# Kernel optimization log

Hardware: AMD Instinct MI355X
Metric: run time of the kernel (lower is better)

## Reference

```python
import jax, jax.numpy as jnp
import numpy as np

DT_SCALER = 1.0 / 24
COVAR_INDEX = np.array([0] + list(range(7, 25)))
INSULIN_INDEX = np.array(list(range(1, 6)))
T = 100          # SEQUENCE_LENGTH
B = 512
H = 256          # hidden_dim
ODE_H = 50       # hidden width of the ODE MLP (hardcoded in cODERNN_)
ODE_STEPS = 8    # fixed-step RK4 stands in for adaptive dopri5 (rtol=atol=1e-3)


def setup_inputs() -> dict:
    key = jax.random.key(0)
    ks = jax.random.split(key, 24)
    std = 0.1
    d = {}
    d["dt"] = jax.random.uniform(ks[0], (B, T, 2), jnp.float32)
    d["x"] = jax.random.normal(ks[1], (B, T, 25), jnp.float32)
    # rnn1: RNNCell(19, H)
    d["Wih1"] = std * jax.random.normal(ks[2], (H, 19), jnp.float32)
    d["Whh1"] = std * jax.random.normal(ks[3], (H, H), jnp.float32)
    d["bih1"] = jnp.zeros((H,), jnp.float32)
    d["bhh1"] = jnp.zeros((H,), jnp.float32)
    # rnn2: RNNCell(5+H, H)
    d["Wih2"] = std * jax.random.normal(ks[4], (H, 5 + H), jnp.float32)
    d["Whh2"] = std * jax.random.normal(ks[5], (H, H), jnp.float32)
    d["bih2"] = jnp.zeros((H,), jnp.float32)
    d["bhh2"] = jnp.zeros((H,), jnp.float32)
    # output_net_covar: Linear(H,H) -> tanh -> Linear(H,1)
    d["oW1"] = std * jax.random.normal(ks[6], (H, H), jnp.float32)
    d["ob1"] = jnp.zeros((H,), jnp.float32)
    d["oW2"] = std * jax.random.normal(ks[7], (1, H), jnp.float32)
    d["ob2"] = jnp.zeros((1,), jnp.float32)
    # output_net_insulin: Linear(H,H) -> tanh -> Linear(H,1) -> relu
    d["iW1"] = std * jax.random.normal(ks[8], (H, H), jnp.float32)
    d["ib1"] = jnp.zeros((H,), jnp.float32)
    d["iW2"] = std * jax.random.normal(ks[9], (1, H), jnp.float32)
    d["ib2"] = jnp.zeros((1,), jnp.float32)
    # ODE func net: Linear(H,50) -> tanh -> Linear(50,H)
    d["fW1"] = std * jax.random.normal(ks[10], (ODE_H, H), jnp.float32)
    d["fb1"] = jnp.zeros((ODE_H,), jnp.float32)
    d["fW2"] = std * jax.random.normal(ks[11], (H, ODE_H), jnp.float32)
    d["fb2"] = jnp.zeros((H,), jnp.float32)
    return d


def _rnn_cell(x, h, Wih, Whh, bih, bhh):
    return jnp.tanh(x @ Wih.T + bih + h @ Whh.T + bhh)


def _solve_ode(h0, scale, fW1, fb1, fW2, fb2):
    """Integrate dh/ds = net(h) * scale over s in [0,1] with fixed-step RK4.
    scale = dt_i * DT_SCALER, shape [B,1]."""
    hs = 1.0 / ODE_STEPS

    def f(h):
        return (jnp.tanh(h @ fW1.T + fb1) @ fW2.T + fb2) * scale

    def step(h, _):
        k1 = f(h)
        k2 = f(h + 0.5 * hs * k1)
        k3 = f(h + 0.5 * hs * k2)
        k4 = f(h + hs * k3)
        return h + (hs / 6.0) * (k1 + 2 * k2 + 2 * k3 + k4), None

    h, _ = jax.lax.scan(step, h0, None, length=ODE_STEPS)
    return h


def reference(dt, x, Wih1, Whh1, bih1, bhh1, Wih2, Whh2, bih2, bhh2,
              oW1, ob1, oW2, ob2, iW1, ib1, iW2, ib2, fW1, fb1, fW2, fb2):
    Bb, Tt, _ = x.shape
    x_ins = x[:, :, INSULIN_INDEX]      # [B,T,5]
    x_cov = x[:, :, COVAR_INDEX]        # [B,T,19]
    treat = (jnp.sum(x_ins > 0, axis=2, keepdims=True) > 0).astype(x.dtype)  # [B,T,1]
    dt_i = (dt[:, :, 1] - dt[:, :, 0])[..., None]                            # [B,T,1]

    def out_cov(h):
        return jnp.tanh(h @ oW1.T + ob1) @ oW2.T + ob2

    def out_ins(h):
        return jax.nn.relu(jnp.tanh(h @ iW1.T + ib1) @ iW2.T + ib2)

    def step(carry, inp):
        h_cov, h_ins = carry
        xc, xi, d, tr = inp             # [B,19],[B,5],[B,1],[B,1]
        h_cov = h_cov + _rnn_cell(xc, h_cov, Wih1, Whh1, bih1, bhh1)
        h_ins = h_ins + _rnn_cell(jnp.concatenate([xi, h_cov], axis=1), h_ins,
                                  Wih2, Whh2, bih2, bhh2)
        scale = d * DT_SCALER
        h_cov = _solve_ode(h_cov, scale, fW1, fb1, fW2, fb2)
        h_ins = _solve_ode(h_ins, scale, fW1, fb1, fW2, fb2)
        mu = out_cov(h_cov) - tr * out_ins(h_ins)   # [B,1]
        return (h_cov, h_ins), mu

    Hd = Whh1.shape[0]
    init = (jnp.zeros((Bb, Hd), x.dtype), jnp.zeros((Bb, Hd), x.dtype))
    xs = (jnp.swapaxes(x_cov, 0, 1), jnp.swapaxes(x_ins, 0, 1),
          jnp.swapaxes(dt_i, 0, 1), jnp.swapaxes(treat, 0, 1))
    _, mus = jax.lax.scan(step, init, xs)           # [T,B,1]
    return jnp.swapaxes(mus[:, :, 0], 0, 1)        # [B,T]
```

## Files before the change

### kernel.cpp

```cpp
#include <hip/hip_runtime.h>

#define TT 100
#define NSTEP 8
__device__ __constant__ float kDT_SC = 1.0f / 24.0f;
#define HS (0.125f)

typedef float f4 __attribute__((ext_vector_type(4)));
typedef float f2 __attribute__((ext_vector_type(2)));

#define OFF_WHH1T4   0
#define OFF_WIH1T    65536
#define OFF_WIH2AT   70656
#define OFF_WIH2BT4  72704
#define OFF_WHH2T4   138240
#define OFF_OW1T4    203776
#define OFF_IW1T4    269312
#define OFF_FW1R     334848
#define OFF_FW2T4    351232
#define OFF_B1C      364544
#define OFF_B2C      364800
#define WS_FLOATS    365056

#define L_FW2   0
#define L_YCUR  13312
#define L_Z     13856
#define L_HC2   13984
#define L_XA    14240
#define L_TR    14268
#define L_RED   14269
#define L_TOTAL 14277

__device__ __forceinline__ float fast_tanh(float v) {
    float e = __expf(2.0f * v);
    return 1.0f - 2.0f / (e + 1.0f);
}
__device__ __forceinline__ f2 vlo(f4 v) { return __builtin_shufflevector(v, v, 0, 1); }
__device__ __forceinline__ f2 vhi(f4 v) { return __builtin_shufflevector(v, v, 2, 3); }
__device__ __forceinline__ void pkfma(f2& a, f2 w, f2 h) {
    a = __builtin_elementwise_fma(w, h, a);
}
__device__ __forceinline__ float rsum2(f2 a) { return a.x + a.y; }

__device__ __forceinline__ int yoffF(int v, int j) { return v * 272 + (j >> 6) * 68 + (j & 63); }
__device__ __forceinline__ int yoff4(int v, int jb) { return v * 68 + (jb >> 4) * 17 + (jb & 15); }

template <int CTRL>
__device__ __forceinline__ float dpp_rr_add(float v) {
    int r = __builtin_amdgcn_update_dpp(0, __float_as_int(v), CTRL, 0xF, 0xF, false);
    return v + __int_as_float(r);
}
__device__ __forceinline__ float allreduce16(float v) {
    v = dpp_rr_add<0x121>(v);
    v = dpp_rr_add<0x122>(v);
    v = dpp_rr_add<0x124>(v);
    v = dpp_rr_add<0x128>(v);
    return v;
}

__global__ void codernn_setup(const float* __restrict__ Wih1, const float* __restrict__ Whh1,
                              const float* __restrict__ bih1, const float* __restrict__ bhh1,
                              const float* __restrict__ Wih2, const float* __restrict__ Whh2,
                              const float* __restrict__ bih2, const float* __restrict__ bhh2,
                              const float* __restrict__ oW1, const float* __restrict__ iW1,
                              const float* __restrict__ fW1, const float* __restrict__ fW2,
                              float* __restrict__ ws) {
    int e = blockIdx.x * 256 + threadIdx.x;
    if (e >= WS_FLOATS) return;
    float v;
    if (e < OFF_WIH1T) {
        int q = e; int jb = q >> 10, i = (q >> 2) & 255, dj = q & 3;
        v = Whh1[i * 256 + jb * 4 + dj];
    } else if (e < OFF_WIH2AT) {
        int q = e - OFF_WIH1T; int j = q >> 8, i = q & 255;
        v = (j < 19) ? Wih1[i * 19 + j] : 0.0f;
    } else if (e < OFF_WIH2BT4) {
        int q = e - OFF_WIH2AT; int j = q >> 8, i = q & 255;
        v = (j < 5) ? Wih2[i * 261 + j] : 0.0f;
    } else if (e < OFF_WHH2T4) {
        int q = e - OFF_WIH2BT4; int jb = q >> 10, i = (q >> 2) & 255, dj = q & 3;
        v = Wih2[i * 261 + 5 + jb * 4 + dj];
    } else if (e < OFF_OW1T4) {
        int q = e - OFF_WHH2T4; int jb = q >> 10, i = (q >> 2) & 255, dj = q & 3;
        v = Whh2[i * 256 + jb * 4 + dj];
    } else if (e < OFF_IW1T4) {
        int q = e - OFF_OW1T4; int jb = q >> 10, i = (q >> 2) & 255, dj = q & 3;
        v = oW1[i * 256 + jb * 4 + dj];
    } else if (e < OFF_FW1R) {
        int q = e - OFF_IW1T4; int jb = q >> 10, i = (q >> 2) & 255, dj = q & 3;
        v = iW1[i * 256 + jb * 4 + dj];
    } else if (e < OFF_FW2T4) {
        int q = e - OFF_FW1R; int k = q >> 8, j = q & 255;
        v = (k < 50) ? fW1[k * 256 + j] : 0.0f;
    } else if (e < OFF_B1C) {
        int q = e - OFF_FW2T4; int kb = q >> 10, i = (q >> 2) & 255, dk = q & 3;
        int k = kb * 4 + dk;
        v = (k < 50) ? fW2[i * 50 + k] : 0.0f;
    } else if (e < OFF_B2C) {
        int q = e - OFF_B1C; v = bih1[q] + bhh1[q];
    } else {
        int q = e - OFF_B2C; v = bih2[q] + bhh2[q];
    }
    ws[e] = v;
}

__global__ __launch_bounds__(256, 2) void codernn_main(
    const float* __restrict__ dt, const float* __restrict__ x,
    const float* __restrict__ ws,
    const float* __restrict__ ob1, const float* __restrict__ oW2, const float* __restrict__ ob2,
    const float* __restrict__ ib1, const float* __restrict__ iW2, const float* __restrict__ ib2,
    const float* __restrict__ fb1, const float* __restrict__ fb2,
    float* __restrict__ out) {
    __shared__ float sm[L_TOTAL];
    const int tid = threadIdx.x;
    const int i = tid;
    const int bg = blockIdx.x;
    const int lane = tid & 63, wv = tid >> 6;

    for (int idx = tid; idx < 13312; idx += 256) sm[L_FW2 + idx] = ws[OFF_FW2T4 + idx];
    for (int idx = tid; idx < 544; idx += 256) sm[L_YCUR + idx] = 0.0f;

    const float b1ci = ws[OFF_B1C + i];
    const float b2ci = ws[OFF_B2C + i];
    const float ob1i = ob1[i], ib1i = ib1[i];
    const float oW2i = oW2[i], iW2i = iW2[i];
    const float fb2i = fb2[i];
    const float ob2s = ob2[0], ib2s = ib2[0];

    const int kg = (tid >> 4) & 15;
    const int p16 = tid & 15;

    const f4* Whh1T4  = (const f4*)(ws + OFF_WHH1T4);
    const float* Wih1T  = ws + OFF_WIH1T;
    const float* Wih2aT = ws + OFF_WIH2AT;
    const f4* Wih2bT4 = (const f4*)(ws + OFF_WIH2BT4);
    const f4* Whh2T4  = (const f4*)(ws + OFF_WHH2T4);
    const f4* oW1T4   = (const f4*)(ws + OFF_OW1T4);
    const f4* iW1T4   = (const f4*)(ws + OFF_IW1T4);
    const f4* ycur4   = (const f4*)(sm + L_YCUR);
    const f4* hc24    = (const f4*)(sm + L_HC2);
    const f4* fw2l    = (const f4*)(sm + L_FW2);

    f4 wz[4][4];
    {
        const f4* g = (const f4*)(ws + OFF_FW1R);
        #pragma unroll
        for (int r = 0; r < 4; ++r)
            #pragma unroll
            for (int m = 0; m < 4; ++m)
                wz[r][m] = g[(4 * kg + r) * 64 + p16 * 4 + m];
    }
    float fb1r[4];
    #pragma unroll
    for (int r = 0; r < 4; ++r) fb1r[r] = (4 * kg + r < 50) ? fb1[4 * kg + r] : 0.0f;

    const int yA = L_YCUR + yoffF(0, i);
    const int yB = L_YCUR + yoffF(1, i);

    float y0a = 0.0f, y0b = 0.0f;
    __syncthreads();

    for (int t = 0; t < TT; ++t) {
        if (tid < 28) {
            sm[L_XA + tid] = (tid < 25) ? x[bg * (TT * 25) + t * 25 + tid] : 0.0f;
        }
        if (i == 0) {
            const float* xp = x + bg * (TT * 25) + t * 25;
            sm[L_TR] = (xp[1] > 0.f || xp[2] > 0.f || xp[3] > 0.f || xp[4] > 0.f || xp[5] > 0.f) ? 1.0f : 0.0f;
        }
        const float sc = (dt[bg * (TT * 2) + t * 2 + 1] - dt[bg * (TT * 2) + t * 2]) * kDT_SC;
        __syncthreads();

        {
            float acc = b1ci;
            acc = fmaf(Wih1T[i], sm[L_XA + 0], acc);
            #pragma unroll
            for (int j = 1; j < 19; ++j)
                acc = fmaf(Wih1T[j * 256 + i], sm[L_XA + 6 + j], acc);
            f2 aL = {0.f, 0.f}, aH = {0.f, 0.f};
            #pragma unroll 4
            for (int jb = 0; jb < 64; ++jb) {
                f4 w = Whh1T4[jb * 256 + i];
                f4 h = ycur4[yoff4(0, jb)];
                pkfma(aL, vlo(w), vlo(h));
                pkfma(aH, vhi(w), vhi(h));
            }
            acc += rsum2(aL + aH);
            y0a = y0a + fast_tanh(acc);
            sm[L_HC2 + i] = y0a;
        }
        __syncthreads();

        {
            float acc = b2ci;
            #pragma unroll
            for (int j = 0; j < 5; ++j)
                acc = fmaf(Wih2aT[j * 256 + i], sm[L_XA + 1 + j], acc);
            f2 aL = {0.f, 0.f}, aH = {0.f, 0.f};
            #pragma unroll 4
            for (int jb = 0; jb < 64; ++jb) {
                f4 w = Wih2bT4[jb * 256 + i];
                f4 h = hc24[jb];
                pkfma(aL, vlo(w), vlo(h));
                pkfma(aH, vhi(w), vhi(h));
            }
            #pragma unroll 4
            for (int jb = 0; jb < 64; ++jb) {
                f4 w = Whh2T4[jb * 256 + i];
                f4 h = ycur4[yoff4(1, jb)];
                pkfma(aL, vlo(w), vlo(h));
                pkfma(aH, vhi(w), vhi(h));
            }
            acc += rsum2(aL + aH);
            y0b = y0b + fast_tanh(acc);
        }
        __syncthreads();
        sm[yA] = y0a;
        sm[yB] = y0b;

        for (int st = 0; st < NSTEP; ++st) {
            float acca = 0.f, accb = 0.f;
            #pragma unroll
            for (int e = 0; e < 4; ++e) {
                __syncthreads();
                float pz[8];
                #pragma unroll
                for (int s = 0; s < 2; ++s) {
                    const f4* ys = ycur4 + s * 68 + (p16 >> 2) * 17 + (p16 & 3) * 4;
                    f2 P0l = {0,0}, P0h = {0,0}, P1l = {0,0}, P1h = {0,0};
                    f2 P2l = {0,0}, P2h = {0,0}, P3l = {0,0}, P3h = {0,0};
                    #pragma unroll
                    for (int m = 0; m < 4; ++m) {
                        f4 y = ys[m];
                        f2 yl = vlo(y), yh = vhi(y);
                        pkfma(P0l, vlo(wz[0][m]), yl); pkfma(P0h, vhi(wz[0][m]), yh);
                        pkfma(P1l, vlo(wz[1][m]), yl); pkfma(P1h, vhi(wz[1][m]), yh);
                        pkfma(P2l, vlo(wz[2][m]), yl); pkfma(P2h, vhi(wz[2][m]), yh);
                        pkfma(P3l, vlo(wz[3][m]), yl); pkfma(P3h, vhi(wz[3][m]), yh);
                    }
                    pz[s * 4 + 0] = rsum2(P0l + P0h);
                    pz[s * 4 + 1] = rsum2(P1l + P1h);
                    pz[s * 4 + 2] = rsum2(P2l + P2h);
                    pz[s * 4 + 3] = rsum2(P3l + P3h);
                }
                #pragma unroll
                for (int r = 0; r < 8; ++r) pz[r] = allreduce16(pz[r]);
                if (p16 < 8) {
                    const int q = p16;
                    float a0 = (q & 1) ? pz[1] : pz[0];
                    float a1 = (q & 1) ? pz[3] : pz[2];
                    float a2 = (q & 1) ? pz[5] : pz[4];
                    float a3 = (q & 1) ? pz[7] : pz[6];
                    float b0s = (q & 2) ? a1 : a0;
                    float b1s = (q & 2) ? a3 : a2;
                    float vsum = (q & 4) ? b1s : b0s;
                    float f0 = (q & 1) ? fb1r[1] : fb1r[0];
                    float f1 = (q & 1) ? fb1r[3] : fb1r[2];
                    float fb = (q & 2) ? f1 : f0;
                    sm[L_Z + (q >> 2) * 64 + 4 * kg + (q & 3)] = fast_tanh(vsum + fb);
                }
                __syncthreads();
                {
                    const f4* zva = (const f4*)(sm + L_Z);
                    const f4* zvb = (const f4*)(sm + L_Z + 64);
                    f2 AL = {0,0}, AH = {0,0}, BL = {0,0}, BH = {0,0};
                    #pragma unroll
                    for (int kb = 0; kb < 13; ++kb) {
                        f4 w = fw2l[kb * 256 + i];
                        f4 za = zva[kb], zb = zvb[kb];
                        pkfma(AL, vlo(w), vlo(za)); pkfma(AH, vhi(w), vhi(za));
                        pkfma(BL, vlo(w), vlo(zb)); pkfma(BH, vhi(w), vhi(zb));
                    }
                    float dua = (fb2i + rsum2(AL + AH)) * sc;
                    float dub = (fb2i + rsum2(BL + BH)) * sc;
                    float ya, yb;
                    if (e == 0) {
                        acca = dua; accb = dub;
                        ya = fmaf(0.5f * HS, dua, y0a); yb = fmaf(0.5f * HS, dub, y0b);
                    } else if (e == 1) {
                        acca = fmaf(2.f, dua, acca); accb = fmaf(2.f, dub, accb);
                        ya = fmaf(0.5f * HS, dua, y0a); yb = fmaf(0.5f * HS, dub, y0b);
                    } else if (e == 2) {
                        acca = fmaf(2.f, dua, acca); accb = fmaf(2.f, dub, accb);
                        ya = fmaf(HS, dua, y0a); yb = fmaf(HS, dub, y0b);
                    } else {
                        acca += dua; accb += dub;
                        y0a = fmaf(HS / 6.f, acca, y0a); y0b = fmaf(HS / 6.f, accb, y0b);
                        ya = y0a; yb = y0b;
                    }
                    sm[yA] = ya;
                    sm[yB] = yb;
                }
            }
        }
        __syncthreads();

        {
            f2 aoL = {0,0}, aoH = {0,0}, aiL = {0,0}, aiH = {0,0};
            #pragma unroll 4
            for (int jb = 0; jb < 64; ++jb) {
                f4 wo = oW1T4[jb * 256 + i];
                f4 hcv = ycur4[yoff4(0, jb)];
                pkfma(aoL, vlo(wo), vlo(hcv)); pkfma(aoH, vhi(wo), vhi(hcv));
                f4 wi = iW1T4[jb * 256 + i];
                f4 hiv = ycur4[yoff4(1, jb)];
                pkfma(aiL, vlo(wi), vlo(hiv)); pkfma(aiH, vhi(wi), vhi(hiv));
            }
            float co = oW2i * fast_tanh(ob1i + rsum2(aoL + aoH));
            float ci = iW2i * fast_tanh(ib1i + rsum2(aiL + aiH));
            #pragma unroll
            for (int off = 32; off > 0; off >>= 1) {
                co += __shfl_xor(co, off);
                ci += __shfl_xor(ci, off);
            }
            if (lane == 0) { sm[L_RED + wv * 2] = co; sm[L_RED + wv * 2 + 1] = ci; }
        }
        __syncthreads();
        if (i == 0) {
            float sco = sm[L_RED + 0] + sm[L_RED + 2] + sm[L_RED + 4] + sm[L_RED + 6];
            float sci = sm[L_RED + 1] + sm[L_RED + 3] + sm[L_RED + 5] + sm[L_RED + 7];
            float muc = sco + ob2s;
            float mui = fmaxf(sci + ib2s, 0.0f);
            out[bg * TT + t] = muc - sm[L_TR] * mui;
        }
        __syncthreads();
    }
}

extern "C" void kernel_launch(void* const* d_in, const int* in_sizes, int n_in,
                              void* d_out, int out_size, void* d_ws, size_t ws_size,
                              hipStream_t stream) {
    const float* dt   = (const float*)d_in[0];
    const float* x    = (const float*)d_in[1];
    const float* Wih1 = (const float*)d_in[2];
    const float* Whh1 = (const float*)d_in[3];
    const float* bih1 = (const float*)d_in[4];
    const float* bhh1 = (const float*)d_in[5];
    const float* Wih2 = (const float*)d_in[6];
    const float* Whh2 = (const float*)d_in[7];
    const float* bih2 = (const float*)d_in[8];
    const float* bhh2 = (const float*)d_in[9];
    const float* oW1  = (const float*)d_in[10];
    const float* ob1  = (const float*)d_in[11];
    const float* oW2  = (const float*)d_in[12];
    const float* ob2  = (const float*)d_in[13];
    const float* iW1  = (const float*)d_in[14];
    const float* ib1  = (const float*)d_in[15];
    const float* iW2  = (const float*)d_in[16];
    const float* ib2  = (const float*)d_in[17];
    const float* fW1  = (const float*)d_in[18];
    const float* fb1  = (const float*)d_in[19];
    const float* fW2  = (const float*)d_in[20];
    const float* fb2  = (const float*)d_in[21];
    float* ws  = (float*)d_ws;
    float* out = (float*)d_out;

    if (ws_size < (size_t)WS_FLOATS * sizeof(float)) return;

    codernn_setup<<<WS_FLOATS / 256, 256, 0, stream>>>(Wih1, Whh1, bih1, bhh1, Wih2, Whh2,
                                                       bih2, bhh2, oW1, iW1, fW1, fW2, ws);

    codernn_main<<<512, 256, 0, stream>>>(dt, x, ws,
                                          ob1, oW2, ob2, ib1, iW2, ib2, fb1, fb2, out);
}
```

Baseline: 5.889 ms.

## Double block to 512 threads, splitting cov and insulin streams across halves

Each block now runs 512 threads. The lower half owns the covariate hidden state and the upper half owns the insulin hidden state for the ODE stages, the RNN matvecs and the output heads. The first RNN matvec is split by K across the two halves and combined through shared-memory partial sums. The goal is more wavefronts per batch row, to hide latency and shorten the serial per-thread work. The cost is extra barriers and partial-sum traffic, and the launch bound changes to (512,4), which caps registers per thread.

```diff
diff --git a/kernel.cpp b/kernel.cpp
--- a/kernel.cpp
+++ b/kernel.cpp
@@ -24,11 +24,11 @@
 #define L_FW2   0
 #define L_YCUR  13312
 #define L_Z     13856
-#define L_HC2   13984
-#define L_XA    14240
-#define L_TR    14268
-#define L_RED   14269
-#define L_TOTAL 14277
+#define L_PART  13984
+#define L_XA    14496
+#define L_TR    14524
+#define L_RED   14525
+#define L_TOTAL 14533
 
 __device__ __forceinline__ float fast_tanh(float v) {
     float e = __expf(2.0f * v);
@@ -103,7 +103,7 @@
     ws[e] = v;
 }
 
-__global__ __launch_bounds__(256, 2) void codernn_main(
+__global__ __launch_bounds__(512, 4) void codernn_main(
     const float* __restrict__ dt, const float* __restrict__ x,
     const float* __restrict__ ws,
     const float* __restrict__ ob1, const float* __restrict__ oW2, const float* __restrict__ ob2,
@@ -112,21 +112,22 @@
     float* __restrict__ out) {
     __shared__ float sm[L_TOTAL];
     const int tid = threadIdx.x;
-    const int i = tid;
+    const int i = tid & 255;
+    const int sh = tid >> 8;
     const int bg = blockIdx.x;
     const int lane = tid & 63, wv = tid >> 6;
 
-    for (int idx = tid; idx < 13312; idx += 256) sm[L_FW2 + idx] = ws[OFF_FW2T4 + idx];
-    for (int idx = tid; idx < 544; idx += 256) sm[L_YCUR + idx] = 0.0f;
+    for (int idx = tid; idx < 13312; idx += 512) sm[L_FW2 + idx] = ws[OFF_FW2T4 + idx];
+    for (int idx = tid; idx < 544; idx += 512) sm[L_YCUR + idx] = 0.0f;
 
     const float b1ci = ws[OFF_B1C + i];
     const float b2ci = ws[OFF_B2C + i];
-    const float ob1i = ob1[i], ib1i = ib1[i];
-    const float oW2i = oW2[i], iW2i = iW2[i];
     const float fb2i = fb2[i];
+    const float W2sel = sh ? iW2[i] : oW2[i];
+    const float b1sel = sh ? ib1[i] : ob1[i];
     const float ob2s = ob2[0], ib2s = ib2[0];
 
-    const int kg = (tid >> 4) & 15;
+    const int kg = tid >> 4;
     const int p16 = tid & 15;
 
     const f4* Whh1T4  = (const f4*)(ws + OFF_WHH1T4);
@@ -137,33 +138,31 @@
     const f4* oW1T4   = (const f4*)(ws + OFF_OW1T4);
     const f4* iW1T4   = (const f4*)(ws + OFF_IW1T4);
     const f4* ycur4   = (const f4*)(sm + L_YCUR);
-    const f4* hc24    = (const f4*)(sm + L_HC2);
     const f4* fw2l    = (const f4*)(sm + L_FW2);
 
-    f4 wz[4][4];
+    f4 wz[2][4];
     {
         const f4* g = (const f4*)(ws + OFF_FW1R);
         #pragma unroll
-        for (int r = 0; r < 4; ++r)
+        for (int r = 0; r < 2; ++r)
             #pragma unroll
             for (int m = 0; m < 4; ++m)
-                wz[r][m] = g[(4 * kg + r) * 64 + p16 * 4 + m];
+                wz[r][m] = g[(2 * kg + r) * 64 + p16 * 4 + m];
     }
-    float fb1r[4];
+    float fb1r[2];
     #pragma unroll
-    for (int r = 0; r < 4; ++r) fb1r[r] = (4 * kg + r < 50) ? fb1[4 * kg + r] : 0.0f;
-
-    const int yA = L_YCUR + yoffF(0, i);
-    const int yB = L_YCUR + yoffF(1, i);
-
-    float y0a = 0.0f, y0b = 0.0f;
+    for (int r = 0; r < 2; ++r) fb1r[r] = (2 * kg + r < 50) ? fb1[2 * kg + r] : 0.0f;
+
+    const int yOwn = L_YCUR + yoffF(sh, i);
+
+    float y0 = 0.0f;
     __syncthreads();
 
     for (int t = 0; t < TT; ++t) {
         if (tid < 28) {
             sm[L_XA + tid] = (tid < 25) ? x[bg * (TT * 25) + t * 25 + tid] : 0.0f;
         }
-        if (i == 0) {
+        if (tid == 28) {
             const float* xp = x + bg * (TT * 25) + t * 25;
             sm[L_TR] = (xp[1] > 0.f || xp[2] > 0.f || xp[3] > 0.f || xp[4] > 0.f || xp[5] > 0.f) ? 1.0f : 0.0f;
         }
@@ -171,156 +170,131 @@
         __syncthreads();
 
         {
-            float acc = b1ci;
-            acc = fmaf(Wih1T[i], sm[L_XA + 0], acc);
-            #pragma unroll
-            for (int j = 1; j < 19; ++j)
-                acc = fmaf(Wih1T[j * 256 + i], sm[L_XA + 6 + j], acc);
+            float acc = 0.0f;
+            if (sh == 0) {
+                acc = fmaf(Wih1T[i], sm[L_XA + 0], b1ci);
+                #pragma unroll
+                for (int j = 1; j < 19; ++j)
+                    acc = fmaf(Wih1T[j * 256 + i], sm[L_XA + 6 + j], acc);
+            }
+            const int jb0 = sh * 32;
+            f2 aL = {0.f, 0.f}, aH = {0.f, 0.f};
+            #pragma unroll 4
+            for (int jb = 0; jb < 32; ++jb) {
+                f4 w = Whh1T4[(jb0 + jb) * 256 + i];
+                f4 h = ycur4[yoff4(0, jb0 + jb)];
+                pkfma(aL, vlo(w), vlo(h));
+                pkfma(aH, vhi(w), vhi(h));
+            }
+            float part = acc + rsum2(aL + aH);
+            sm[L_PART + sh * 256 + i] = part;
+            __syncthreads();
+            if (sh == 0) {
+                y0 = y0 + fast_tanh(part + sm[L_PART + 256 + i]);
+                sm[L_YCUR + yoffF(0, i)] = y0;
+            }
+        }
+        __syncthreads();
+
+        {
+            float acc = 0.0f;
+            if (sh == 0) {
+                acc = b2ci;
+                #pragma unroll
+                for (int j = 0; j < 5; ++j)
+                    acc = fmaf(Wih2aT[j * 256 + i], sm[L_XA + 1 + j], acc);
+            }
+            const f4* Wp = sh ? Whh2T4 : Wih2bT4;
             f2 aL = {0.f, 0.f}, aH = {0.f, 0.f};
             #pragma unroll 4
             for (int jb = 0; jb < 64; ++jb) {
-                f4 w = Whh1T4[jb * 256 + i];
-                f4 h = ycur4[yoff4(0, jb)];
+                f4 w = Wp[jb * 256 + i];
+                f4 h = ycur4[yoff4(sh, jb)];
                 pkfma(aL, vlo(w), vlo(h));
                 pkfma(aH, vhi(w), vhi(h));
             }
-            acc += rsum2(aL + aH);
-            y0a = y0a + fast_tanh(acc);
-            sm[L_HC2 + i] = y0a;
-        }
-        __syncthreads();
-
-        {
-            float acc = b2ci;
-            #pragma unroll
-            for (int j = 0; j < 5; ++j)
-                acc = fmaf(Wih2aT[j * 256 + i], sm[L_XA + 1 + j], acc);
-            f2 aL = {0.f, 0.f}, aH = {0.f, 0.f};
-            #pragma unroll 4
-            for (int jb = 0; jb < 64; ++jb) {
-                f4 w = Wih2bT4[jb * 256 + i];
-                f4 h = hc24[jb];
-                pkfma(aL, vlo(w), vlo(h));
-                pkfma(aH, vhi(w), vhi(h));
-            }
-            #pragma unroll 4
-            for (int jb = 0; jb < 64; ++jb) {
-                f4 w = Whh2T4[jb * 256 + i];
-                f4 h = ycur4[yoff4(1, jb)];
-                pkfma(aL, vlo(w), vlo(h));
-                pkfma(aH, vhi(w), vhi(h));
-            }
-            acc += rsum2(aL + aH);
-            y0b = y0b + fast_tanh(acc);
-        }
-        __syncthreads();
-        sm[yA] = y0a;
-        sm[yB] = y0b;
+            float part = acc + rsum2(aL + aH);
+            sm[L_PART + sh * 256 + i] = part;
+            __syncthreads();
+            if (sh == 1) {
+                y0 = y0 + fast_tanh(sm[L_PART + i] + part);
+                sm[L_YCUR + yoffF(1, i)] = y0;
+            }
+        }
 
         for (int st = 0; st < NSTEP; ++st) {
-            float acca = 0.f, accb = 0.f;
+            float acc_rk = 0.0f;
             #pragma unroll
             for (int e = 0; e < 4; ++e) {
                 __syncthreads();
-                float pz[8];
+                float pz[4];
                 #pragma unroll
                 for (int s = 0; s < 2; ++s) {
                     const f4* ys = ycur4 + s * 68 + (p16 >> 2) * 17 + (p16 & 3) * 4;
                     f2 P0l = {0,0}, P0h = {0,0}, P1l = {0,0}, P1h = {0,0};
-                    f2 P2l = {0,0}, P2h = {0,0}, P3l = {0,0}, P3h = {0,0};
                     #pragma unroll
                     for (int m = 0; m < 4; ++m) {
                         f4 y = ys[m];
                         f2 yl = vlo(y), yh = vhi(y);
                         pkfma(P0l, vlo(wz[0][m]), yl); pkfma(P0h, vhi(wz[0][m]), yh);
                         pkfma(P1l, vlo(wz[1][m]), yl); pkfma(P1h, vhi(wz[1][m]), yh);
-                        pkfma(P2l, vlo(wz[2][m]), yl); pkfma(P2h, vhi(wz[2][m]), yh);
-                        pkfma(P3l, vlo(wz[3][m]), yl); pkfma(P3h, vhi(wz[3][m]), yh);
                     }
-                    pz[s * 4 + 0] = rsum2(P0l + P0h);
-                    pz[s * 4 + 1] = rsum2(P1l + P1h);
-                    pz[s * 4 + 2] = rsum2(P2l + P2h);
-                    pz[s * 4 + 3] = rsum2(P3l + P3h);
+                    pz[s * 2 + 0] = rsum2(P0l + P0h);
+                    pz[s * 2 + 1] = rsum2(P1l + P1h);
                 }
                 #pragma unroll
-                for (int r = 0; r < 8; ++r) pz[r] = allreduce16(pz[r]);
-                if (p16 < 8) {
+                for (int r = 0; r < 4; ++r) pz[r] = allreduce16(pz[r]);
+                if (p16 < 4) {
                     const int q = p16;
                     float a0 = (q & 1) ? pz[1] : pz[0];
                     float a1 = (q & 1) ? pz[3] : pz[2];
-                    float a2 = (q & 1) ? pz[5] : pz[4];
-                    float a3 = (q & 1) ? pz[7] : pz[6];
-                    float b0s = (q & 2) ? a1 : a0;
-                    float b1s = (q & 2) ? a3 : a2;
-                    float vsum = (q & 4) ? b1s : b0s;
-                    float f0 = (q & 1) ? fb1r[1] : fb1r[0];
-                    float f1 = (q & 1) ? fb1r[3] : fb1r[2];
-                    float fb = (q & 2) ? f1 : f0;
-                    sm[L_Z + (q >> 2) * 64 + 4 * kg + (q & 3)] = fast_tanh(vsum + fb);
+                    float vv = (q & 2) ? a1 : a0;
+                    float fbs = (q & 1) ? fb1r[1] : fb1r[0];
+                    sm[L_Z + (q >> 1) * 64 + 2 * kg + (q & 1)] = fast_tanh(vv + fbs);
                 }
                 __syncthreads();
                 {
-                    const f4* zva = (const f4*)(sm + L_Z);
-                    const f4* zvb = (const f4*)(sm + L_Z + 64);
-                    f2 AL = {0,0}, AH = {0,0}, BL = {0,0}, BH = {0,0};
+                    const f4* zv = (const f4*)(sm + L_Z + sh * 64);
+                    f2 AL = {0,0}, AH = {0,0};
                     #pragma unroll
                     for (int kb = 0; kb < 13; ++kb) {
                         f4 w = fw2l[kb * 256 + i];
-                        f4 za = zva[kb], zb = zvb[kb];
-                        pkfma(AL, vlo(w), vlo(za)); pkfma(AH, vhi(w), vhi(za));
-                        pkfma(BL, vlo(w), vlo(zb)); pkfma(BH, vhi(w), vhi(zb));
+                        f4 z = zv[kb];
+                        pkfma(AL, vlo(w), vlo(z));
+                        pkfma(AH, vhi(w), vhi(z));
                     }
-                    float dua = (fb2i + rsum2(AL + AH)) * sc;
-                    float dub = (fb2i + rsum2(BL + BH)) * sc;
-                    float ya, yb;
-                    if (e == 0) {
-                        acca = dua; accb = dub;
-                        ya = fmaf(0.5f * HS, dua, y0a); yb = fmaf(0.5f * HS, dub, y0b);
-                    } else if (e == 1) {
-                        acca = fmaf(2.f, dua, acca); accb = fmaf(2.f, dub, accb);
-                        ya = fmaf(0.5f * HS, dua, y0a); yb = fmaf(0.5f * HS, dub, y0b);
-                    } else if (e == 2) {
-                        acca = fmaf(2.f, dua, acca); accb = fmaf(2.f, dub, accb);
-                        ya = fmaf(HS, dua, y0a); yb = fmaf(HS, dub, y0b);
-                    } else {
-                        acca += dua; accb += dub;
-                        y0a = fmaf(HS / 6.f, acca, y0a); y0b = fmaf(HS / 6.f, accb, y0b);
-                        ya = y0a; yb = y0b;
-                    }
-                    sm[yA] = ya;
-                    sm[yB] = yb;
+                    float du = (fb2i + rsum2(AL + AH)) * sc;
+                    float yn;
+                    if (e == 0) { acc_rk = du; yn = fmaf(0.5f * HS, du, y0); }
+                    else if (e == 1) { acc_rk = fmaf(2.f, du, acc_rk); yn = fmaf(0.5f * HS, du, y0); }
+                    else if (e == 2) { acc_rk = fmaf(2.f, du, acc_rk); yn = fmaf(HS, du, y0); }
+                    else { acc_rk += du; y0 = fmaf(HS / 6.f, acc_rk, y0); yn = y0; }
+                    sm[yOwn] = yn;
                 }
             }
         }
         __syncthreads();
 
         {
-            f2 aoL = {0,0}, aoH = {0,0}, aiL = {0,0}, aiH = {0,0};
+            const f4* Wh = sh ? iW1T4 : oW1T4;
+            f2 aL = {0,0}, aH = {0,0};
             #pragma unroll 4
             for (int jb = 0; jb < 64; ++jb) {
-                f4 wo = oW1T4[jb * 256 + i];
-                f4 hcv = ycur4[yoff4(0, jb)];
-                pkfma(aoL, vlo(wo), vlo(hcv)); pkfma(aoH, vhi(wo), vhi(hcv));
-                f4 wi = iW1T4[jb * 256 + i];
-                f4 hiv = ycur4[yoff4(1, jb)];
-                pkfma(aiL, vlo(wi), vlo(hiv)); pkfma(aiH, vhi(wi), vhi(hiv));
-            }
-            float co = oW2i * fast_tanh(ob1i + rsum2(aoL + aoH));
-            float ci = iW2i * fast_tanh(ib1i + rsum2(aiL + aiH));
+                f4 w = Wh[jb * 256 + i];
+                f4 h = ycur4[yoff4(sh, jb)];
+                pkfma(aL, vlo(w), vlo(h));
+                pkfma(aH, vhi(w), vhi(h));
+            }
+            float val = W2sel * fast_tanh(b1sel + rsum2(aL + aH));
             #pragma unroll
-            for (int off = 32; off > 0; off >>= 1) {
-                co += __shfl_xor(co, off);
-                ci += __shfl_xor(ci, off);
-            }
-            if (lane == 0) { sm[L_RED + wv * 2] = co; sm[L_RED + wv * 2 + 1] = ci; }
-        }
-        __syncthreads();
-        if (i == 0) {
-            float sco = sm[L_RED + 0] + sm[L_RED + 2] + sm[L_RED + 4] + sm[L_RED + 6];
-            float sci = sm[L_RED + 1] + sm[L_RED + 3] + sm[L_RED + 5] + sm[L_RED + 7];
-            float muc = sco + ob2s;
-            float mui = fmaxf(sci + ib2s, 0.0f);
-            out[bg * TT + t] = muc - sm[L_TR] * mui;
+            for (int off = 32; off > 0; off >>= 1) val += __shfl_xor(val, off);
+            if (lane == 0) sm[L_RED + wv] = val;
+        }
+        __syncthreads();
+        if (tid == 0) {
+            float co = sm[L_RED + 0] + sm[L_RED + 1] + sm[L_RED + 2] + sm[L_RED + 3] + ob2s;
+            float ci = sm[L_RED + 4] + sm[L_RED + 5] + sm[L_RED + 6] + sm[L_RED + 7] + ib2s;
+            out[bg * TT + t] = co - sm[L_TR] * fmaxf(ci, 0.0f);
         }
         __syncthreads();
     }
@@ -359,6 +333,6 @@
     codernn_setup<<<WS_FLOATS / 256, 256, 0, stream>>>(Wih1, Whh1, bih1, bhh1, Wih2, Whh2,
                                                        bih2, bhh2, oW1, iW1, fW1, fW2, ws);
 
-    codernn_main<<<512, 256, 0, stream>>>(dt, x, ws,
+    codernn_main<<<512, 512, 0, stream>>>(dt, x, ws,
                                           ob1, oW2, ob2, ib1, iW2, ib2, fb1, fb2, out);
 }
```

Result: slower. 17.24 ms (+192.7%).

## Split each sample across 512 threads with specialized halves and register-cached ODE weights

Applied to the files above, without the earlier changes.

Doubles the block to 512 threads so that two 256-thread halves share each batch row. The RNN matvecs are split by K or by operand between the halves, combined through a shared partial buffer. In the ODE stage, half 0 computes the first MLP layer while half 1 computes the second layer, using fW2 held in registers instead of a large shared-memory copy. This shrinks shared memory and spreads the serial per-sample work over more waves, but adds barriers and leaves half the threads idle during each ODE sub-stage.

```diff
diff --git a/kernel.cpp b/kernel.cpp
--- a/kernel.cpp
+++ b/kernel.cpp
@@ -21,14 +21,13 @@
 #define OFF_B2C      364800
 #define WS_FLOATS    365056
 
-#define L_FW2   0
-#define L_YCUR  13312
-#define L_Z     13856
-#define L_HC2   13984
-#define L_XA    14240
-#define L_TR    14268
-#define L_RED   14269
-#define L_TOTAL 14277
+#define L_YCUR  0
+#define L_Z     544
+#define L_PART  672
+#define L_XA    928
+#define L_TR    956
+#define L_RED   957
+#define L_TOTAL 965
 
 __device__ __forceinline__ float fast_tanh(float v) {
     float e = __expf(2.0f * v);
@@ -103,7 +102,7 @@
     ws[e] = v;
 }
 
-__global__ __launch_bounds__(256, 2) void codernn_main(
+__global__ __launch_bounds__(512, 2) void codernn_main(
     const float* __restrict__ dt, const float* __restrict__ x,
     const float* __restrict__ ws,
     const float* __restrict__ ob1, const float* __restrict__ oW2, const float* __restrict__ ob2,
@@ -112,18 +111,18 @@
     float* __restrict__ out) {
     __shared__ float sm[L_TOTAL];
     const int tid = threadIdx.x;
-    const int i = tid;
+    const int i = tid & 255;
+    const int sh = tid >> 8;
     const int bg = blockIdx.x;
     const int lane = tid & 63, wv = tid >> 6;
 
-    for (int idx = tid; idx < 13312; idx += 256) sm[L_FW2 + idx] = ws[OFF_FW2T4 + idx];
-    for (int idx = tid; idx < 544; idx += 256) sm[L_YCUR + idx] = 0.0f;
+    for (int idx = tid; idx < 544; idx += 512) sm[L_YCUR + idx] = 0.0f;
 
     const float b1ci = ws[OFF_B1C + i];
     const float b2ci = ws[OFF_B2C + i];
-    const float ob1i = ob1[i], ib1i = ib1[i];
-    const float oW2i = oW2[i], iW2i = iW2[i];
     const float fb2i = fb2[i];
+    const float W2sel = sh ? iW2[i] : oW2[i];
+    const float b1sel = sh ? ib1[i] : ob1[i];
     const float ob2s = ob2[0], ib2s = ib2[0];
 
     const int kg = (tid >> 4) & 15;
@@ -137,17 +136,21 @@
     const f4* oW1T4   = (const f4*)(ws + OFF_OW1T4);
     const f4* iW1T4   = (const f4*)(ws + OFF_IW1T4);
     const f4* ycur4   = (const f4*)(sm + L_YCUR);
-    const f4* hc24    = (const f4*)(sm + L_HC2);
-    const f4* fw2l    = (const f4*)(sm + L_FW2);
-
-    f4 wz[4][4];
-    {
+
+    f4 cache[16];
+    if (sh == 0) {
         const f4* g = (const f4*)(ws + OFF_FW1R);
         #pragma unroll
         for (int r = 0; r < 4; ++r)
             #pragma unroll
             for (int m = 0; m < 4; ++m)
-                wz[r][m] = g[(4 * kg + r) * 64 + p16 * 4 + m];
+                cache[r * 4 + m] = g[(4 * kg + r) * 64 + p16 * 4 + m];
+    } else {
+        const f4* g = (const f4*)(ws + OFF_FW2T4);
+        #pragma unroll
+        for (int kb = 0; kb < 13; ++kb)
+            cache[kb] = g[kb * 256 + i];
+        cache[13] = (f4){0,0,0,0}; cache[14] = (f4){0,0,0,0}; cache[15] = (f4){0,0,0,0};
     }
     float fb1r[4];
     #pragma unroll
@@ -163,109 +166,118 @@
         if (tid < 28) {
             sm[L_XA + tid] = (tid < 25) ? x[bg * (TT * 25) + t * 25 + tid] : 0.0f;
         }
-        if (i == 0) {
+        if (tid == 28) {
             const float* xp = x + bg * (TT * 25) + t * 25;
             sm[L_TR] = (xp[1] > 0.f || xp[2] > 0.f || xp[3] > 0.f || xp[4] > 0.f || xp[5] > 0.f) ? 1.0f : 0.0f;
         }
         const float sc = (dt[bg * (TT * 2) + t * 2 + 1] - dt[bg * (TT * 2) + t * 2]) * kDT_SC;
         __syncthreads();
 
+        float part;
         {
-            float acc = b1ci;
-            acc = fmaf(Wih1T[i], sm[L_XA + 0], acc);
-            #pragma unroll
-            for (int j = 1; j < 19; ++j)
-                acc = fmaf(Wih1T[j * 256 + i], sm[L_XA + 6 + j], acc);
+            float acc = 0.0f;
+            if (sh == 0) {
+                acc = fmaf(Wih1T[i], sm[L_XA + 0], b1ci);
+                #pragma unroll
+                for (int j = 1; j < 19; ++j)
+                    acc = fmaf(Wih1T[j * 256 + i], sm[L_XA + 6 + j], acc);
+            }
+            const int jb0 = sh * 32;
+            f2 aL = {0.f, 0.f}, aH = {0.f, 0.f};
+            #pragma unroll 4
+            for (int jb = 0; jb < 32; ++jb) {
+                f4 w = Whh1T4[(jb0 + jb) * 256 + i];
+                f4 h = ycur4[yoff4(0, jb0 + jb)];
+                pkfma(aL, vlo(w), vlo(h));
+                pkfma(aH, vhi(w), vhi(h));
+            }
+            part = acc + rsum2(aL + aH);
+            if (sh == 0) sm[L_PART + i] = part;
+        }
+        __syncthreads();
+        if (sh == 1) {
+            y0a = y0a + fast_tanh(sm[L_PART + i] + part);
+            sm[yA] = y0a;
+        }
+        __syncthreads();
+
+        {
+            float acc = 0.0f;
+            if (sh == 0) {
+                acc = b2ci;
+                #pragma unroll
+                for (int j = 0; j < 5; ++j)
+                    acc = fmaf(Wih2aT[j * 256 + i], sm[L_XA + 1 + j], acc);
+            }
+            const f4* Wp = sh ? Whh2T4 : Wih2bT4;
             f2 aL = {0.f, 0.f}, aH = {0.f, 0.f};
             #pragma unroll 4
             for (int jb = 0; jb < 64; ++jb) {
-                f4 w = Whh1T4[jb * 256 + i];
-                f4 h = ycur4[yoff4(0, jb)];
+                f4 w = Wp[jb * 256 + i];
+                f4 h = ycur4[yoff4(sh, jb)];
                 pkfma(aL, vlo(w), vlo(h));
                 pkfma(aH, vhi(w), vhi(h));
             }
-            acc += rsum2(aL + aH);
-            y0a = y0a + fast_tanh(acc);
-            sm[L_HC2 + i] = y0a;
-        }
-        __syncthreads();
-
-        {
-            float acc = b2ci;
-            #pragma unroll
-            for (int j = 0; j < 5; ++j)
-                acc = fmaf(Wih2aT[j * 256 + i], sm[L_XA + 1 + j], acc);
-            f2 aL = {0.f, 0.f}, aH = {0.f, 0.f};
-            #pragma unroll 4
-            for (int jb = 0; jb < 64; ++jb) {
-                f4 w = Wih2bT4[jb * 256 + i];
-                f4 h = hc24[jb];
-                pkfma(aL, vlo(w), vlo(h));
-                pkfma(aH, vhi(w), vhi(h));
-            }
-            #pragma unroll 4
-            for (int jb = 0; jb < 64; ++jb) {
-                f4 w = Whh2T4[jb * 256 + i];
-                f4 h = ycur4[yoff4(1, jb)];
-                pkfma(aL, vlo(w), vlo(h));
-                pkfma(aH, vhi(w), vhi(h));
-            }
-            acc += rsum2(aL + aH);
-            y0b = y0b + fast_tanh(acc);
-        }
-        __syncthreads();
-        sm[yA] = y0a;
-        sm[yB] = y0b;
+            part = acc + rsum2(aL + aH);
+            if (sh == 0) sm[L_PART + i] = part;
+        }
+        __syncthreads();
+        if (sh == 1) {
+            y0b = y0b + fast_tanh(sm[L_PART + i] + part);
+            sm[yB] = y0b;
+        }
 
         for (int st = 0; st < NSTEP; ++st) {
             float acca = 0.f, accb = 0.f;
             #pragma unroll
             for (int e = 0; e < 4; ++e) {
                 __syncthreads();
-                float pz[8];
-                #pragma unroll
-                for (int s = 0; s < 2; ++s) {
-                    const f4* ys = ycur4 + s * 68 + (p16 >> 2) * 17 + (p16 & 3) * 4;
-                    f2 P0l = {0,0}, P0h = {0,0}, P1l = {0,0}, P1h = {0,0};
-                    f2 P2l = {0,0}, P2h = {0,0}, P3l = {0,0}, P3h = {0,0};
+                if (sh == 0) {
+                    float pz[8];
                     #pragma unroll
-                    for (int m = 0; m < 4; ++m) {
-                        f4 y = ys[m];
-                        f2 yl = vlo(y), yh = vhi(y);
-                        pkfma(P0l, vlo(wz[0][m]), yl); pkfma(P0h, vhi(wz[0][m]), yh);
-                        pkfma(P1l, vlo(wz[1][m]), yl); pkfma(P1h, vhi(wz[1][m]), yh);
-                        pkfma(P2l, vlo(wz[2][m]), yl); pkfma(P2h, vhi(wz[2][m]), yh);
-                        pkfma(P3l, vlo(wz[3][m]), yl); pkfma(P3h, vhi(wz[3][m]), yh);
+                    for (int s = 0; s < 2; ++s) {
+                        const f4* ys = ycur4 + s * 68 + (p16 >> 2) * 17 + (p16 & 3) * 4;
+                        f2 P0l = {0,0}, P0h = {0,0}, P1l = {0,0}, P1h = {0,0};
+                        f2 P2l = {0,0}, P2h = {0,0}, P3l = {0,0}, P3h = {0,0};
+                        #pragma unroll
+                        for (int m = 0; m < 4; ++m) {
+                            f4 y = ys[m];
+                            f2 yl = vlo(y), yh = vhi(y);
+                            pkfma(P0l, vlo(cache[m]), yl);      pkfma(P0h, vhi(cache[m]), yh);
+                            pkfma(P1l, vlo(cache[4 + m]), yl);  pkfma(P1h, vhi(cache[4 + m]), yh);
+                            pkfma(P2l, vlo(cache[8 + m]), yl);  pkfma(P2h, vhi(cache[8 + m]), yh);
+                            pkfma(P3l, vlo(cache[12 + m]), yl); pkfma(P3h, vhi(cache[12 + m]), yh);
+                        }
+                        pz[s * 4 + 0] = rsum2(P0l + P0h);
+                        pz[s * 4 + 1] = rsum2(P1l + P1h);
+                        pz[s * 4 + 2] = rsum2(P2l + P2h);
+                        pz[s * 4 + 3] = rsum2(P3l + P3h);
                     }
-                    pz[s * 4 + 0] = rsum2(P0l + P0h);
-                    pz[s * 4 + 1] = rsum2(P1l + P1h);
-                    pz[s * 4 + 2] = rsum2(P2l + P2h);
-                    pz[s * 4 + 3] = rsum2(P3l + P3h);
-                }
-                #pragma unroll
-                for (int r = 0; r < 8; ++r) pz[r] = allreduce16(pz[r]);
-                if (p16 < 8) {
-                    const int q = p16;
-                    float a0 = (q & 1) ? pz[1] : pz[0];
-                    float a1 = (q & 1) ? pz[3] : pz[2];
-                    float a2 = (q & 1) ? pz[5] : pz[4];
-                    float a3 = (q & 1) ? pz[7] : pz[6];
-                    float b0s = (q & 2) ? a1 : a0;
-                    float b1s = (q & 2) ? a3 : a2;
-                    float vsum = (q & 4) ? b1s : b0s;
-                    float f0 = (q & 1) ? fb1r[1] : fb1r[0];
-                    float f1 = (q & 1) ? fb1r[3] : fb1r[2];
-                    float fb = (q & 2) ? f1 : f0;
-                    sm[L_Z + (q >> 2) * 64 + 4 * kg + (q & 3)] = fast_tanh(vsum + fb);
+                    #pragma unroll
+                    for (int r = 0; r < 8; ++r) pz[r] = allreduce16(pz[r]);
+                    if (p16 < 8) {
+                        const int q = p16;
+                        float a0 = (q & 1) ? pz[1] : pz[0];
+                        float a1 = (q & 1) ? pz[3] : pz[2];
+                        float a2 = (q & 1) ? pz[5] : pz[4];
+                        float a3 = (q & 1) ? pz[7] : pz[6];
+                        float b0s = (q & 2) ? a1 : a0;
+                        float b1s = (q & 2) ? a3 : a2;
+                        float vsum = (q & 4) ? b1s : b0s;
+                        float f0 = (q & 1) ? fb1r[1] : fb1r[0];
+                        float f1 = (q & 1) ? fb1r[3] : fb1r[2];
+                        float fb = (q & 2) ? f1 : f0;
+                        sm[L_Z + (q >> 2) * 64 + 4 * kg + (q & 3)] = fast_tanh(vsum + fb);
+                    }
                 }
                 __syncthreads();
-                {
+                if (sh == 1) {
                     const f4* zva = (const f4*)(sm + L_Z);
                     const f4* zvb = (const f4*)(sm + L_Z + 64);
                     f2 AL = {0,0}, AH = {0,0}, BL = {0,0}, BH = {0,0};
                     #pragma unroll
                     for (int kb = 0; kb < 13; ++kb) {
-                        f4 w = fw2l[kb * 256 + i];
+                        f4 w = cache[kb];
                         f4 za = zva[kb], zb = zvb[kb];
                         pkfma(AL, vlo(w), vlo(za)); pkfma(AH, vhi(w), vhi(za));
                         pkfma(BL, vlo(w), vlo(zb)); pkfma(BH, vhi(w), vhi(zb));
@@ -295,32 +307,25 @@
         __syncthreads();
 
         {
-            f2 aoL = {0,0}, aoH = {0,0}, aiL = {0,0}, aiH = {0,0};
+            const f4* Wh = sh ? iW1T4 : oW1T4;
+            f2 aL = {0,0}, aH = {0,0};
             #pragma unroll 4
             for (int jb = 0; jb < 64; ++jb) {
-                f4 wo = oW1T4[jb * 256 + i];
-                f4 hcv = ycur4[yoff4(0, jb)];
-                pkfma(aoL, vlo(wo), vlo(hcv)); pkfma(aoH, vhi(wo), vhi(hcv));
-                f4 wi = iW1T4[jb * 256 + i];
-                f4 hiv = ycur4[yoff4(1, jb)];
-                pkfma(aiL, vlo(wi), vlo(hiv)); pkfma(aiH, vhi(wi), vhi(hiv));
-            }
-            float co = oW2i * fast_tanh(ob1i + rsum2(aoL + aoH));
-            float ci = iW2i * fast_tanh(ib1i + rsum2(aiL + aiH));
+                f4 w = Wh[jb * 256 + i];
+                f4 h = ycur4[yoff4(sh, jb)];
+                pkfma(aL, vlo(w), vlo(h));
+                pkfma(aH, vhi(w), vhi(h));
+            }
+            float val = W2sel * fast_tanh(b1sel + rsum2(aL + aH));
             #pragma unroll
-            for (int off = 32; off > 0; off >>= 1) {
-                co += __shfl_xor(co, off);
-                ci += __shfl_xor(ci, off);
-            }
-            if (lane == 0) { sm[L_RED + wv * 2] = co; sm[L_RED + wv * 2 + 1] = ci; }
-        }
-        __syncthreads();
-        if (i == 0) {
-            float sco = sm[L_RED + 0] + sm[L_RED + 2] + sm[L_RED + 4] + sm[L_RED + 6];
-            float sci = sm[L_RED + 1] + sm[L_RED + 3] + sm[L_RED + 5] + sm[L_RED + 7];
-            float muc = sco + ob2s;
-            float mui = fmaxf(sci + ib2s, 0.0f);
-            out[bg * TT + t] = muc - sm[L_TR] * mui;
+            for (int off = 32; off > 0; off >>= 1) val += __shfl_xor(val, off);
+            if (lane == 0) sm[L_RED + wv] = val;
+        }
+        __syncthreads();
+        if (tid == 0) {
+            float co = sm[L_RED + 0] + sm[L_RED + 1] + sm[L_RED + 2] + sm[L_RED + 3] + ob2s;
+            float ci = sm[L_RED + 4] + sm[L_RED + 5] + sm[L_RED + 6] + sm[L_RED + 7] + ib2s;
+            out[bg * TT + t] = co - sm[L_TR] * fmaxf(ci, 0.0f);
         }
         __syncthreads();
     }
@@ -359,6 +364,6 @@
     codernn_setup<<<WS_FLOATS / 256, 256, 0, stream>>>(Wih1, Whh1, bih1, bhh1, Wih2, Whh2,
                                                        bih2, bhh2, oW1, iW1, fW1, fW2, ws);
 
-    codernn_main<<<512, 256, 0, stream>>>(dt, x, ws,
+    codernn_main<<<512, 512, 0, stream>>>(dt, x, ws,
                                           ob1, oW2, ob2, ib1, iW2, ib2, fb1, fb2, out);
 }
```

After: 8.011 ms. +36.0%, slower.
